# Performance work log

Measured on AMD Instinct MI355X. Metric: run time of the kernel, lower is better.

The kernel has to match this reference:

```python
import jax, jax.numpy as jnp
import numpy as np
from jax import lax

N_IMG = 2
LEVEL_HW = [(200, 200), (100, 100), (50, 50), (25, 25), (13, 13)]
STRIDES = [4, 8, 16, 32, 64]
SIZES = [32.0, 64.0, 128.0, 256.0, 512.0]
A = 3
LEVEL_SIZES = [A * h * w for h, w in LEVEL_HW]
R = sum(LEVEL_SIZES)  # 159882
PRE_NMS = 1000   # pre_nms_top_n['testing']
POST_NMS = 1000  # post_nms_top_n['testing']
NMS_THRESH = 0.7
SCORE_THRESH = 0.0
MIN_SIZE = 1e-3
IMG_H = IMG_W = 800.0
BBOX_XFORM_CLIP = float(np.log(1000.0 / 16.0))


def _make_anchors():
    ratios = np.array([0.5, 1.0, 2.0])
    h_r = np.sqrt(ratios)
    w_r = 1.0 / h_r
    out = []
    for (h, w), stride, size in zip(LEVEL_HW, STRIDES, SIZES):
        ws = size * w_r
        hs = size * h_r
        base = np.stack([-ws / 2, -hs / 2, ws / 2, hs / 2], 1)  # [A,4]
        sx = (np.arange(w) + 0.5) * stride
        sy = (np.arange(h) + 0.5) * stride
        yy, xx = np.meshgrid(sy, sx, indexing='ij')
        shifts = np.stack([xx.ravel(), yy.ravel(), xx.ravel(), yy.ravel()], 1)  # [H*W,4]
        out.append((shifts[:, None, :] + base[None, :, :]).reshape(-1, 4))
    return np.concatenate(out, 0).astype(np.float32)  # [R,4]


def setup_inputs() -> dict:
    key = jax.random.key(0)
    k1, k2 = jax.random.split(key)
    objectness = jax.random.normal(k1, (N_IMG, R), jnp.float32)
    deltas = jax.random.normal(k2, (N_IMG, R, 4), jnp.float32) * 0.2
    anchors = jnp.asarray(_make_anchors())
    return {"objectness": objectness, "deltas": deltas, "anchors": anchors}


def _decode(deltas, anchors):
    # BoxCoder.decode with weights (1,1,1,1)
    wa = anchors[:, 2] - anchors[:, 0]
    ha = anchors[:, 3] - anchors[:, 1]
    cxa = anchors[:, 0] + 0.5 * wa
    cya = anchors[:, 1] + 0.5 * ha
    dx, dy, dw, dh = deltas[..., 0], deltas[..., 1], deltas[..., 2], deltas[..., 3]
    dw = jnp.minimum(dw, BBOX_XFORM_CLIP)
    dh = jnp.minimum(dh, BBOX_XFORM_CLIP)
    cx = dx * wa + cxa
    cy = dy * ha + cya
    w = jnp.exp(dw) * wa
    h = jnp.exp(dh) * ha
    return jnp.stack([cx - 0.5 * w, cy - 0.5 * h, cx + 0.5 * w, cy + 0.5 * h], -1)


def _nms_single(boxes, scores, lvl, valid):
    # batched_nms via per-level coordinate offset trick
    offs = lvl.astype(boxes.dtype) * (max(IMG_H, IMG_W) + 1.0)
    ob = boxes + offs[:, None]
    s = jnp.where(valid, scores, -1.0)
    order = jnp.argsort(-s)
    b = ob[order]          # offset boxes, score-descending
    raw = boxes[order]     # original boxes
    v = valid[order]
    ss = s[order]
    area = (b[:, 2] - b[:, 0]) * (b[:, 3] - b[:, 1])
    lt = jnp.maximum(b[:, None, :2], b[None, :, :2])
    rb = jnp.minimum(b[:, None, 2:], b[None, :, 2:])
    wh = jnp.clip(rb - lt, 0.0)
    inter = wh[..., 0] * wh[..., 1]
    iou = inter / (area[:, None] + area[None, :] - inter + 1e-9)  # [K,K]
    K = b.shape[0]

    def body(keep, i):
        suppressed = jnp.any(keep & (iou[:, i] > NMS_THRESH))
        keep = keep.at[i].set(v[i] & ~suppressed)
        return keep, None

    keep, _ = lax.scan(body, jnp.zeros((K,), bool), jnp.arange(K))
    # compact kept boxes (score order preserved) into fixed POST_NMS slots
    pos = jnp.where(keep, jnp.minimum(jnp.cumsum(keep) - 1, POST_NMS), POST_NMS)
    out_b = jnp.zeros((POST_NMS + 1, 4), boxes.dtype).at[pos].set(raw)[:POST_NMS]
    out_s = jnp.full((POST_NMS + 1,), -1.0, boxes.dtype).at[pos].set(ss)[:POST_NMS]
    return out_b, out_s


def _forward(objectness, deltas, anchors):
    proposals = _decode(deltas, anchors)  # [N,R,4]
    # per-level topk (pre_nms_top_n)
    idxs = []
    off = 0
    for n in LEVEL_SIZES:
        k = min(PRE_NMS, n)
        _, ti = lax.top_k(objectness[:, off:off + n], k)
        idxs.append(ti + off)
        off += n
    top_idx = jnp.concatenate(idxs, 1)  # [N,K]
    obj = jnp.take_along_axis(objectness, top_idx, 1)
    boxes = jnp.take_along_axis(proposals, top_idx[..., None], 1)
    levels = jnp.concatenate([jnp.full((n,), i, jnp.int32) for i, n in enumerate(LEVEL_SIZES)])
    lvl = levels[top_idx]
    scores = jax.nn.sigmoid(obj)
    # clip_boxes_to_image
    x1 = jnp.clip(boxes[..., 0], 0.0, IMG_W)
    y1 = jnp.clip(boxes[..., 1], 0.0, IMG_H)
    x2 = jnp.clip(boxes[..., 2], 0.0, IMG_W)
    y2 = jnp.clip(boxes[..., 3], 0.0, IMG_H)
    boxes = jnp.stack([x1, y1, x2, y2], -1)
    # remove_small_boxes + score_thresh -> validity mask (fixed shapes)
    valid = (x2 - x1 >= MIN_SIZE) & (y2 - y1 >= MIN_SIZE) & (scores >= SCORE_THRESH)
    return jax.vmap(_nms_single)(boxes, scores, lvl, valid)


def reference(objectness, deltas, anchors):
    return _forward(objectness, deltas, anchors)
```

## Files before the change

### kernel.cpp

```cpp
#include <hip/hip_runtime.h>

typedef unsigned long long u64;
typedef unsigned int u32;

#define R_TOT 159882
#define POST 1000
#define IMG_SZ 800.0f
#define NMS_TH 0.7f
#define BBOX_CLIP 4.135166556742356f
#define LCAP 1024

__device__ __forceinline__ float fadd_(float a, float b){ return __fadd_rn(a,b); }
__device__ __forceinline__ float fsub_(float a, float b){ return __fsub_rn(a,b); }
__device__ __forceinline__ float fmul_(float a, float b){ return __fmul_rn(a,b); }

__device__ __forceinline__ int lvl_len(int l){ const int L[5]={120000,30000,7500,1875,507}; return L[l]; }
__device__ __forceinline__ int lvl_off(int l){ const int L[5]={0,120000,150000,157500,159375}; return L[l]; }
__device__ __forceinline__ int lvl_k(int l){ const int L[5]={1000,1000,1000,1000,507}; return L[l]; }

__device__ __forceinline__ u32 mono_(u32 u){ return (u & 0x80000000u) ? ~u : (u | 0x80000000u); }

__device__ __forceinline__ u64 readlane64(u64 v, int i){
  u32 lo = (u32)__builtin_amdgcn_readlane((int)(u32)v, i);
  u32 hi = (u32)__builtin_amdgcn_readlane((int)(u32)(v >> 32), i);
  return ((u64)hi << 32) | (u64)lo;
}

__global__ __launch_bounds__(256) void k_hist(const float* __restrict__ obj, int* hist16){
  int g = blockIdx.x, sl = blockIdx.y;
  int img = g/5, lvl = g%5;
  int n = lvl_len(lvl), s0 = lvl_off(lvl);
  __shared__ int lh[4096];
  int tid = threadIdx.x;
  for (int i = tid; i < 4096; i += 256) lh[i] = 0;
  __syncthreads();
  int lo = (int)((long long)n * sl / 16), hiS = (int)((long long)n * (sl+1) / 16);
  const float* p = obj + img*R_TOT + s0;
  #pragma unroll 4
  for (int e = lo + tid; e < hiS; e += 256){
    u32 mu = mono_(__float_as_uint(p[e]));
    atomicAdd(&lh[(~mu) >> 20], 1);
  }
  __syncthreads();
  int* dst = hist16 + (g*16 + sl)*4096;
  for (int i = tid; i < 4096; i += 256) dst[i] = lh[i];
}

__global__ __launch_bounds__(256) void k_collect(const float* __restrict__ obj,
                                                 const int* __restrict__ hist16,
                                                 u64* mainS, u64* tieS,
                                                 int* cntS, int* cnt2S,
                                                 int* bstarG, int* remG){
  int g = blockIdx.x, sl = blockIdx.y;
  int img = g/5, lvl = g%5;
  int n = lvl_len(lvl), s0 = lvl_off(lvl), k = lvl_k(lvl);
  int tid = threadIdx.x, lane = tid & 63, wid = tid >> 6;
  __shared__ int wsum[4];
  __shared__ int sh_bs, sh_rem, lc, lc2;
  __shared__ u64 lmain[1024];
  __shared__ u64 lbuf2[1024];

  int h[16];
  #pragma unroll
  for (int j = 0; j < 16; j++) h[j] = 0;
  const int* hb = hist16 + g*16*4096 + 16*tid;
  for (int s2 = 0; s2 < 16; s2++){
    const int4* hs = (const int4*)(hb + s2*4096);
    int4 a = hs[0], b = hs[1], c = hs[2], d = hs[3];
    h[0]+=a.x;  h[1]+=a.y;  h[2]+=a.z;  h[3]+=a.w;
    h[4]+=b.x;  h[5]+=b.y;  h[6]+=b.z;  h[7]+=b.w;
    h[8]+=c.x;  h[9]+=c.y;  h[10]+=c.z; h[11]+=c.w;
    h[12]+=d.x; h[13]+=d.y; h[14]+=d.z; h[15]+=d.w;
  }
  int part = 0;
  #pragma unroll
  for (int j = 0; j < 16; j++) part += h[j];
  int x = part;
  for (int d = 1; d < 64; d <<= 1){ int y = __shfl_up(x, d); if (lane >= d) x += y; }
  if (lane == 63) wsum[wid] = x;
  if (tid == 0){ lc = 0; lc2 = 0; }
  __syncthreads();
  int add = 0;
  for (int w = 0; w < wid; w++) add += wsum[w];
  int incl = x + add, excl = incl - part;
  if (excl < k && k <= incl){
    int cum = excl;
    #pragma unroll
    for (int q = 0; q < 16; q++){
      if (cum + h[q] >= k){ sh_bs = 16*tid + q; sh_rem = k - cum; break; }
      cum += h[q];
    }
  }
  __syncthreads();
  int bs = sh_bs;
  if (sl == 0 && tid == 0){ bstarG[g] = bs; remG[g] = sh_rem; }

  int lo = (int)((long long)n * sl / 16), hiS = (int)((long long)n * (sl+1) / 16);
  const float* p = obj + img*R_TOT + s0;
  #pragma unroll 4
  for (int e = lo + tid; e < hiS; e += 256){
    u32 mu = mono_(__float_as_uint(p[e]));
    u64 key56 = (((u64)(~mu)) << 24) | (u32)(s0 + e);
    int bin = (int)(key56 >> 44);
    if (bin < bs){ int pos = atomicAdd(&lc, 1); lmain[pos] = key56; }
    else if (bin == bs){ int pos = atomicAdd(&lc2, 1); if (pos < 1024) lbuf2[pos] = key56; }
  }
  __syncthreads();
  int idx16 = g*16 + sl;
  if (tid == 0){ cntS[idx16] = lc; cnt2S[idx16] = lc2; }
  for (int i = tid; i < lc; i += 256) mainS[idx16*1024 + i] = lmain[i];
  int c2l = lc2 < 1024 ? lc2 : 1024;
  for (int i = tid; i < c2l; i += 256) tieS[idx16*1024 + i] = lbuf2[i];
}

__global__ __launch_bounds__(1024) void k_seldecode(const float* __restrict__ obj,
                                                    const float4* __restrict__ deltas,
                                                    const float4* __restrict__ anchors,
                                                    const u64* __restrict__ mainS,
                                                    const u64* __restrict__ tieS,
                                                    const int* __restrict__ cntS,
                                                    const int* __restrict__ cnt2S,
                                                    const int* __restrict__ remG,
                                                    const int* __restrict__ bstarG,
                                                    float4* boxL, float* scoreL,
                                                    float4* nbox, u64* okeyN, int* ncnt){
  int g = blockIdx.x, img = g/5, lvl = g%5;
  int s0 = lvl_off(lvl), n = lvl_len(lvl), k = lvl_k(lvl);
  const float* p = obj + img*R_TOT + s0;
  __shared__ u64 Lbuf[LCAP];
  __shared__ u64 mainL[1024];
  __shared__ float4 lbox[1024];
  __shared__ u64 lokey[1024];
  __shared__ unsigned char lval[1024];
  __shared__ int h16[16];
  __shared__ int scnt[16], tcnt[16];
  __shared__ int sbase[17], tbase[17];
  __shared__ int sh_sc, sh_rem;
  __shared__ u64 sh_thr;
  int tid = threadIdx.x, lane = tid & 63;
  if (tid < 16){ scnt[tid] = cntS[g*16 + tid]; tcnt[tid] = cnt2S[g*16 + tid]; }
  __syncthreads();
  if (tid == 0){
    int s = 0, t2 = 0;
    #pragma unroll
    for (int q = 0; q < 16; q++){ sbase[q] = s; s += scnt[q]; tbase[q] = t2; t2 += tcnt[q]; }
    sbase[16] = s; tbase[16] = t2;
  }
  __syncthreads();
  int nb = sbase[16];
  int c2 = tbase[16];
  int rem = remG[g];
  int bs = bstarG[g];
  {
    u64 vmain = ~0ull;
    if (tid < nb){
      int sl = 0;
      #pragma unroll
      for (int q = 1; q < 16; q++) sl += (tid >= sbase[q]) ? 1 : 0;
      vmain = mainS[(g*16 + sl)*1024 + (tid - sbase[sl])];
    }
    mainL[tid] = vmain;
  }
  if (tid == 0){ sh_sc = 0; sh_rem = rem; }
  int c2c = c2 < LCAP ? c2 : LCAP;
  for (int e = tid; e < c2c; e += 1024){
    int sl = 0;
    #pragma unroll
    for (int q = 1; q < 16; q++) sl += (e >= tbase[q]) ? 1 : 0;
    Lbuf[e] = tieS[(g*16 + sl)*1024 + (e - tbase[sl])];
  }
  __syncthreads();
  if (c2 <= LCAP){
    for (int e = tid; e < c2; e += 1024){
      u64 kk = Lbuf[e];
      int rk = 0;
      for (int q = 0; q < c2; q++) rk += (Lbuf[q] < kk) ? 1 : 0;
      if (rk < rem){ int p2 = atomicAdd(&sh_sc, 1); mainL[nb + p2] = kk; }
    }
  } else {
    if (tid == 0) sh_thr = ((u64)bs) << 44;
    __syncthreads();
    for (int shift = 40; shift >= 0; shift -= 4){
      if (tid < 16) h16[tid] = 0;
      __syncthreads();
      u64 pref = sh_thr;
      u64 himask = ~((1ull << (shift+4)) - 1ull);
      for (int e = tid; e < n; e += 1024){
        u32 mu = mono_(__float_as_uint(p[e]));
        u64 kk = (((u64)(~mu)) << 24) | (u32)(s0 + e);
        if ((kk & himask) == (pref & himask)) atomicAdd(&h16[(int)((kk >> shift) & 15)], 1);
      }
      __syncthreads();
      if (tid == 0){
        int r2 = sh_rem, cum = 0;
        for (int d = 0; d < 16; d++){
          int hb = h16[d];
          if (cum + hb >= r2){ sh_thr = pref | ((u64)d << shift); sh_rem = r2 - cum; break; }
          cum += hb;
        }
      }
      __syncthreads();
    }
    u64 thr = sh_thr;
    for (int e = tid; e < n; e += 1024){
      u32 mu = mono_(__float_as_uint(p[e]));
      u64 kk = (((u64)(~mu)) << 24) | (u32)(s0 + e);
      if ((int)(kk >> 44) == bs && kk <= thr){ int p2 = atomicAdd(&sh_sc, 1); mainL[nb + p2] = kk; }
    }
  }
  __syncthreads();
  for (int k2 = 2; k2 <= 1024; k2 <<= 1){
    for (int j = k2 >> 1; j > 0; j >>= 1){
      __syncthreads();
      int i = tid, ixj = i ^ j;
      if (ixj > i){
        u64 a = mainL[i], b = mainL[ixj];
        bool up = (i & k2) == 0;
        if ((a > b) == up){ mainL[i] = b; mainL[ixj] = a; }
      }
    }
  }
  __syncthreads();
  int r = tid, t = g*1024 + r;
  if (r < k){
    int idx = (int)(mainL[r] & 0xFFFFFFu);
    float4 a = anchors[idx];
    float4 d = deltas[img*R_TOT + idx];
    float o = obj[img*R_TOT + idx];
    float wa = fsub_(a.z, a.x), ha = fsub_(a.w, a.y);
    float cxa = fadd_(a.x, fmul_(0.5f, wa)), cya = fadd_(a.y, fmul_(0.5f, ha));
    float dw = fminf(d.z, BBOX_CLIP), dh = fminf(d.w, BBOX_CLIP);
    float cx = fadd_(fmul_(d.x, wa), cxa), cy = fadd_(fmul_(d.y, ha), cya);
    float w  = fmul_(expf(dw), wa),        h  = fmul_(expf(dh), ha);
    float x1 = fsub_(cx, fmul_(0.5f, w)), y1 = fsub_(cy, fmul_(0.5f, h));
    float x2 = fadd_(cx, fmul_(0.5f, w)), y2 = fadd_(cy, fmul_(0.5f, h));
    x1 = fminf(fmaxf(x1, 0.0f), IMG_SZ); y1 = fminf(fmaxf(y1, 0.0f), IMG_SZ);
    x2 = fminf(fmaxf(x2, 0.0f), IMG_SZ); y2 = fminf(fmaxf(y2, 0.0f), IMG_SZ);
    bool valid = (fsub_(x2, x1) >= 1e-3f) && (fsub_(y2, y1) >= 1e-3f);
    float e = expf(-o);
    float sig = __fdiv_rn(1.0f, fadd_(1.0f, e));
    float s = valid ? sig : -1.0f;
    u32 sb = __float_as_uint(s);
    u32 ms = (sb & 0x80000000u) ? ~sb : (sb | 0x80000000u);
    float4 b4 = make_float4(x1, y1, x2, y2);
    boxL[t] = b4;
    scoreL[t] = sig;
    lokey[r] = (((u64)(~ms)) << 32) | (u32)(lvl*1000 + r);
    lbox[r] = b4;
    lval[r] = valid ? 1 : 0;
  } else {
    lval[r] = 0;
  }
  __syncthreads();
  if (tid < 64){
    int cnt = 0;
    float off = (float)lvl * 801.0f;
    for (int base = 0; base < k; base += 64){
      int r2 = base + lane;
      bool v = (r2 < k) && lval[r2];
      float4 b = lbox[r2 < k ? r2 : 0];
      u64 mask = __ballot(v);
      int before = __popcll(mask & ((1ull << lane) - 1ull));
      if (v){
        int pos = cnt + before;
        nbox[g*1024 + pos] = make_float4(fadd_(b.x,off), fadd_(b.y,off), fadd_(b.z,off), fadd_(b.w,off));
        okeyN[g*1024 + pos] = lokey[r2];
      }
      cnt += __popcll(mask);
    }
    if (lane == 0) ncnt[g] = cnt;
  }
}

__global__ __launch_bounds__(64) void k_mask(const float4* __restrict__ nbox,
                                             const int* __restrict__ ncnt,
                                             u64* LTG2){
  int g = blockIdx.x, tr = blockIdx.y, tw = blockIdx.z;
  if (tw > tr) return;
  int m = ncnt[g];
  if (tr*64 >= m) return;
  __shared__ float4 shb[64];
  __shared__ float sharea[64];
  int lane = threadIdx.x;
  if (tw*64 + lane < m){
    float4 b = nbox[g*1024 + tw*64 + lane];
    shb[lane] = b;
    sharea[lane] = fmul_(fsub_(b.z,b.x), fsub_(b.w,b.y));
  }
  __syncthreads();
  int j = tr*64 + lane;
  if (j >= m) return;
  float4 a = nbox[g*1024 + j];
  float areaA = fmul_(fsub_(a.z,a.x), fsub_(a.w,a.y));
  int imax = m - tw*64; if (imax > 64) imax = 64;
  if (tw == tr){
    u64 bitsF = 0;
    for (int ii = lane+1; ii < imax; ii++){
      float4 b = shb[ii];
      float ltx = fmaxf(a.x, b.x), lty = fmaxf(a.y, b.y);
      float rbx = fminf(a.z, b.z), rby = fminf(a.w, b.w);
      float wx = fmaxf(fsub_(rbx, ltx), 0.0f), wy = fmaxf(fsub_(rby, lty), 0.0f);
      float inter = fmul_(wx, wy);
      float den = fadd_(fsub_(fadd_(areaA, sharea[ii]), inter), 1e-9f);
      if (__fdiv_rn(inter, den) > NMS_TH) bitsF |= (1ull << ii);
    }
    LTG2[((size_t)(g*1024 + j))*16 + 15] = bitsF;
  } else {
    u64 bits = 0;
    for (int ii = 0; ii < imax; ii++){
      float4 b = shb[ii];
      float ltx = fmaxf(a.x, b.x), lty = fmaxf(a.y, b.y);
      float rbx = fminf(a.z, b.z), rby = fminf(a.w, b.w);
      float wx = fmaxf(fsub_(rbx, ltx), 0.0f), wy = fmaxf(fsub_(rby, lty), 0.0f);
      float inter = fmul_(wx, wy);
      float den = fadd_(fsub_(fadd_(areaA, sharea[ii]), inter), 1e-9f);
      if (__fdiv_rn(inter, den) > NMS_TH) bits |= (1ull << ii);
    }
    LTG2[((size_t)(g*1024 + j))*16 + tw] = bits;
  }
}

struct ChunkBuf {
  ulonglong2 v0, v1, v2, v3, v4, v5, v6, v7;
  u64 ok;
};

__device__ __forceinline__ void issue_chunk(const u64* __restrict__ LT2,
                                            const u64* __restrict__ oK,
                                            int c, int lane, ChunkBuf& b){
  int row = c*64 + lane;
  const ulonglong2* rp = (const ulonglong2*)(LT2 + (size_t)row*16);
  b.v0 = rp[0]; b.v1 = rp[1]; b.v2 = rp[2]; b.v3 = rp[3];
  b.v4 = rp[4]; b.v5 = rp[5]; b.v6 = rp[6]; b.v7 = rp[7];
  b.ok = oK[row];
}

__device__ __forceinline__ void consume_chunk(const ChunkBuf& b, int c, int m, int lane,
                                              u64* KwR, u64* runsL, int& cnt){
  int row = c*64 + lane;
  bool inr = row < m;
  u64 supp = 0;
  #define TERM(q, val) supp |= (((q) < c) ? (val) : 0ull) & KwR[q];
  TERM(0,  b.v0.x) TERM(1,  b.v0.y) TERM(2,  b.v1.x) TERM(3,  b.v1.y)
  TERM(4,  b.v2.x) TERM(5,  b.v2.y) TERM(6,  b.v3.x) TERM(7,  b.v3.y)
  TERM(8,  b.v4.x) TERM(9,  b.v4.y) TERM(10, b.v5.x) TERM(11, b.v5.y)
  TERM(12, b.v6.x) TERM(13, b.v6.y) TERM(14, b.v7.x)
  #undef TERM
  u64 fwd = inr ? b.v7.y : 0;
  u64 live = __ballot(inr && (supp == 0));
  u64 fz = __ballot(fwd != 0);
  u64 kept = 0;
  while (1){
    u64 lf = live & fz;
    if (!lf){ kept |= live; break; }
    int i = __builtin_ctzll(lf);
    u64 bi = 1ull << i;
    u64 below = live & (bi - 1ull);
    kept |= below | bi;
    live &= ~(below | bi);
    live &= ~readlane64(fwd, i);
  }
  KwR[c] = kept;
  bool kp = (kept >> lane) & 1ull;
  int before = __popcll(kept & ((1ull << lane) - 1ull));
  if (kp) runsL[cnt + before] = b.ok;
  cnt += __popcll(kept);
}

__global__ __launch_bounds__(1024) void k_scanmerge(const u64* __restrict__ LTG2,
                                                    const int* __restrict__ ncnt,
                                                    const u64* __restrict__ okeyN,
                                                    const float4* __restrict__ boxL,
                                                    const float* __restrict__ scoreL,
                                                    float* out){
  int img = blockIdx.x, tid = threadIdx.x, lane = tid & 63, wid = tid >> 6;
  __shared__ u64 runs[5*1024];
  __shared__ u64 Kw[5][16];
  __shared__ int cl[5];
  if (wid < 5){
    int l = wid, g = img*5 + l;
    int m = ncnt[g];
    int nch = (m + 63) >> 6;
    const u64* LT2 = LTG2 + ((size_t)g*1024)*16;
    const u64* oK = okeyN + g*1024;
    u64* KwR = &Kw[l][0];
    u64* runsL = &runs[l*1024];
    int cnt = 0;
    ChunkBuf A, B;
    if (nch > 0){
      issue_chunk(LT2, oK, 0, lane, A);
      int c = 0;
      while (c < nch){
        if (c+1 < nch) issue_chunk(LT2, oK, c+1, lane, B);
        consume_chunk(A, c, m, lane, KwR, runsL, cnt);
        c++;
        if (c >= nch) break;
        if (c+1 < nch) issue_chunk(LT2, oK, c+1, lane, A);
        consume_chunk(B, c, m, lane, KwR, runsL, cnt);
        c++;
      }
    }
    if (lane == 0) cl[l] = cnt;
  } else {
    for (int t = tid - 320; t < POST; t += 704){
      out[img*POST*4 + t*4 + 0] = 0.0f;
      out[img*POST*4 + t*4 + 1] = 0.0f;
      out[img*POST*4 + t*4 + 2] = 0.0f;
      out[img*POST*4 + t*4 + 3] = 0.0f;
      out[2*POST*4 + img*POST + t] = -1.0f;
    }
  }
  __syncthreads();
  for (int idx = tid; idx < 5*1024; idx += 1024){
    int l = idx >> 10, i = idx & 1023;
    if (i < cl[l]){
      u64 key = runs[l*1024 + i];
      int o0 = l+1; if (o0 >= 5) o0 -= 5;
      int o1 = l+2; if (o1 >= 5) o1 -= 5;
      int o2 = l+3; if (o2 >= 5) o2 -= 5;
      int o3 = l+4; if (o3 >= 5) o3 -= 5;
      const u64* r0 = runs + (o0 << 10);
      const u64* r1 = runs + (o1 << 10);
      const u64* r2 = runs + (o2 << 10);
      const u64* r3 = runs + (o3 << 10);
      int lo0 = 0, hi0 = cl[o0];
      int lo1 = 0, hi1 = cl[o1];
      int lo2 = 0, hi2 = cl[o2];
      int lo3 = 0, hi3 = cl[o3];
      #pragma unroll 1
      for (int st = 0; st < 11; st++){
        int m0 = (lo0+hi0)>>1, m1 = (lo1+hi1)>>1, m2 = (lo2+hi2)>>1, m3 = (lo3+hi3)>>1;
        u64 a0 = r0[m0], a1 = r1[m1], a2 = r2[m2], a3 = r3[m3];
        if (lo0 < hi0){ if (a0 < key) lo0 = m0+1; else hi0 = m0; }
        if (lo1 < hi1){ if (a1 < key) lo1 = m1+1; else hi1 = m1; }
        if (lo2 < hi2){ if (a2 < key) lo2 = m2+1; else hi2 = m2; }
        if (lo3 < hi3){ if (a3 < key) lo3 = m3+1; else hi3 = m3; }
      }
      int rank = i + lo0 + lo1 + lo2 + lo3;
      if (rank < POST){
        int pos = (int)(key & 0xFFFFFFFFull);
        int lvl = pos / 1000, r = pos - lvl*1000;
        int gg = img*5 + lvl;
        float4 bo = boxL[gg*1024 + r];
        float sc = scoreL[gg*1024 + r];
        out[img*POST*4 + rank*4 + 0] = bo.x;
        out[img*POST*4 + rank*4 + 1] = bo.y;
        out[img*POST*4 + rank*4 + 2] = bo.z;
        out[img*POST*4 + rank*4 + 3] = bo.w;
        out[2*POST*4 + img*POST + rank] = sc;
      }
    }
  }
}

extern "C" void kernel_launch(void* const* d_in, const int* in_sizes, int n_in,
                              void* d_out, int out_size, void* d_ws, size_t ws_size,
                              hipStream_t stream){
  (void)in_sizes; (void)n_in; (void)out_size; (void)ws_size;
  const float*  obj     = (const float*)d_in[0];
  const float4* deltas  = (const float4*)d_in[1];
  const float4* anchors = (const float4*)d_in[2];
  float* out = (float*)d_out;
  char* ws = (char*)d_ws;
  int* hist16  = (int*)(ws + 0);
  u64* mainS   = (u64*)(ws + 2621440);
  u64* tieS    = (u64*)(ws + 3932160);
  int* cntS    = (int*)(ws + 5242880);
  int* cnt2S   = (int*)(ws + 5243520);
  int* bstarG  = (int*)(ws + 5244160);
  int* remG    = (int*)(ws + 5244224);
  float4* boxL = (float4*)(ws + 5244288);
  float* scoreL= (float*)(ws + 5408128);
  u64* okeyN   = (u64*)(ws + 5449088);
  float4* nbox = (float4*)(ws + 5531008);
  u64* LTG2    = (u64*)(ws + 5694848);
  int* ncnt    = (int*)(ws + 7005568);

  {
    dim3 gh(10, 16);
    k_hist<<<gh, 256, 0, stream>>>(obj, hist16);
  }
  {
    dim3 gc(10, 16);
    k_collect<<<gc, 256, 0, stream>>>(obj, hist16, mainS, tieS, cntS, cnt2S, bstarG, remG);
  }
  k_seldecode<<<10, 1024, 0, stream>>>(obj, deltas, anchors, mainS, tieS, cntS, cnt2S,
                                       remG, bstarG, boxL, scoreL, nbox, okeyN, ncnt);
  {
    dim3 gm(10, 16, 16);
    k_mask<<<gm, 64, 0, stream>>>(nbox, ncnt, LTG2);
  }
  k_scanmerge<<<2, 1024, 0, stream>>>(LTG2, ncnt, okeyN, boxL, scoreL, out);
}
```

Before: 157.7 us.

## Fuse histogram and collect kernels using per-slice local top-k threshold

Merges k_hist and k_collect into a single k_front kernel. Each slice now picks its own threshold bin from its local histogram, keeping its top min(k, slice size) candidates, so no global histogram round trip through memory is needed. k_seldecode then re-histograms the gathered candidates to find the global bin and remainder. It falls back to a full-level radix select when tie buffers overflow. This removes a kernel launch and the 16x4096 histogram write and read, at the cost of more candidates per level being moved and sorted in the select kernel.

```diff
diff --git a/kernel.cpp b/kernel.cpp
--- a/kernel.cpp
+++ b/kernel.cpp
@@ -26,15 +26,21 @@
   return ((u64)hi << 32) | (u64)lo;
 }
 
-__global__ __launch_bounds__(256) void k_hist(const float* __restrict__ obj, int* hist16){
+__global__ __launch_bounds__(256) void k_front(const float* __restrict__ obj,
+                                               u64* mainS, u64* tieS,
+                                               int* cntS, int* cnt2S){
   int g = blockIdx.x, sl = blockIdx.y;
   int img = g/5, lvl = g%5;
-  int n = lvl_len(lvl), s0 = lvl_off(lvl);
-  __shared__ int lh[4096];
-  int tid = threadIdx.x;
+  int n = lvl_len(lvl), s0 = lvl_off(lvl), k = lvl_k(lvl);
+  int tid = threadIdx.x, lane = tid & 63, wid = tid >> 6;
+  __shared__ __align__(16) int lh[4096];
+  __shared__ int wsum[4];
+  __shared__ int sh_bs, lc, lc2;
   for (int i = tid; i < 4096; i += 256) lh[i] = 0;
   __syncthreads();
   int lo = (int)((long long)n * sl / 16), hiS = (int)((long long)n * (sl+1) / 16);
+  int ns = hiS - lo;
+  int ks = k < ns ? k : ns;
   const float* p = obj + img*R_TOT + s0;
   #pragma unroll 4
   for (int e = lo + tid; e < hiS; e += 256){
@@ -42,36 +48,9 @@
     atomicAdd(&lh[(~mu) >> 20], 1);
   }
   __syncthreads();
-  int* dst = hist16 + (g*16 + sl)*4096;
-  for (int i = tid; i < 4096; i += 256) dst[i] = lh[i];
-}
-
-__global__ __launch_bounds__(256) void k_collect(const float* __restrict__ obj,
-                                                 const int* __restrict__ hist16,
-                                                 u64* mainS, u64* tieS,
-                                                 int* cntS, int* cnt2S,
-                                                 int* bstarG, int* remG){
-  int g = blockIdx.x, sl = blockIdx.y;
-  int img = g/5, lvl = g%5;
-  int n = lvl_len(lvl), s0 = lvl_off(lvl), k = lvl_k(lvl);
-  int tid = threadIdx.x, lane = tid & 63, wid = tid >> 6;
-  __shared__ int wsum[4];
-  __shared__ int sh_bs, sh_rem, lc, lc2;
-  __shared__ u64 lmain[1024];
-  __shared__ u64 lbuf2[1024];
-
   int h[16];
   #pragma unroll
-  for (int j = 0; j < 16; j++) h[j] = 0;
-  const int* hb = hist16 + g*16*4096 + 16*tid;
-  for (int s2 = 0; s2 < 16; s2++){
-    const int4* hs = (const int4*)(hb + s2*4096);
-    int4 a = hs[0], b = hs[1], c = hs[2], d = hs[3];
-    h[0]+=a.x;  h[1]+=a.y;  h[2]+=a.z;  h[3]+=a.w;
-    h[4]+=b.x;  h[5]+=b.y;  h[6]+=b.z;  h[7]+=b.w;
-    h[8]+=c.x;  h[9]+=c.y;  h[10]+=c.z; h[11]+=c.w;
-    h[12]+=d.x; h[13]+=d.y; h[14]+=d.z; h[15]+=d.w;
-  }
+  for (int j = 0; j < 16; j++) h[j] = lh[16*tid + j];
   int part = 0;
   #pragma unroll
   for (int j = 0; j < 16; j++) part += h[j];
@@ -83,34 +62,32 @@
   int add = 0;
   for (int w = 0; w < wid; w++) add += wsum[w];
   int incl = x + add, excl = incl - part;
-  if (excl < k && k <= incl){
+  if (excl < ks && ks <= incl){
     int cum = excl;
     #pragma unroll
     for (int q = 0; q < 16; q++){
-      if (cum + h[q] >= k){ sh_bs = 16*tid + q; sh_rem = k - cum; break; }
+      if (cum + h[q] >= ks){ sh_bs = 16*tid + q; break; }
       cum += h[q];
     }
   }
   __syncthreads();
   int bs = sh_bs;
-  if (sl == 0 && tid == 0){ bstarG[g] = bs; remG[g] = sh_rem; }
-
-  int lo = (int)((long long)n * sl / 16), hiS = (int)((long long)n * (sl+1) / 16);
-  const float* p = obj + img*R_TOT + s0;
+  u64* lmain = (u64*)lh;
+  u64* ltie  = (u64*)lh + 1024;
   #pragma unroll 4
   for (int e = lo + tid; e < hiS; e += 256){
     u32 mu = mono_(__float_as_uint(p[e]));
     u64 key56 = (((u64)(~mu)) << 24) | (u32)(s0 + e);
     int bin = (int)(key56 >> 44);
     if (bin < bs){ int pos = atomicAdd(&lc, 1); lmain[pos] = key56; }
-    else if (bin == bs){ int pos = atomicAdd(&lc2, 1); if (pos < 1024) lbuf2[pos] = key56; }
+    else if (bin == bs){ int pos = atomicAdd(&lc2, 1); if (pos < 1024) ltie[pos] = key56; }
   }
   __syncthreads();
   int idx16 = g*16 + sl;
   if (tid == 0){ cntS[idx16] = lc; cnt2S[idx16] = lc2; }
   for (int i = tid; i < lc; i += 256) mainS[idx16*1024 + i] = lmain[i];
   int c2l = lc2 < 1024 ? lc2 : 1024;
-  for (int i = tid; i < c2l; i += 256) tieS[idx16*1024 + i] = lbuf2[i];
+  for (int i = tid; i < c2l; i += 256) tieS[idx16*1024 + i] = ltie[i];
 }
 
 __global__ __launch_bounds__(1024) void k_seldecode(const float* __restrict__ obj,
@@ -120,8 +97,6 @@
                                                     const u64* __restrict__ tieS,
                                                     const int* __restrict__ cntS,
                                                     const int* __restrict__ cnt2S,
-                                                    const int* __restrict__ remG,
-                                                    const int* __restrict__ bstarG,
                                                     float4* boxL, float* scoreL,
                                                     float4* nbox, u64* okeyN, int* ncnt){
   int g = blockIdx.x, img = g/5, lvl = g%5;
@@ -129,56 +104,146 @@
   const float* p = obj + img*R_TOT + s0;
   __shared__ u64 Lbuf[LCAP];
   __shared__ u64 mainL[1024];
-  __shared__ float4 lbox[1024];
+  __shared__ __align__(16) float4 lbox[1024];
   __shared__ u64 lokey[1024];
   __shared__ unsigned char lval[1024];
   __shared__ int h16[16];
   __shared__ int scnt[16], tcnt[16];
   __shared__ int sbase[17], tbase[17];
-  __shared__ int sh_sc, sh_rem;
+  __shared__ int wsum16[16];
+  __shared__ int sh_bs, sh_rem, sh_mc, sh_tc, sh_sc, sh_rem2, sh_ovf;
   __shared__ u64 sh_thr;
-  int tid = threadIdx.x, lane = tid & 63;
+  int tid = threadIdx.x, lane = tid & 63, wid = tid >> 6;
+  int* chist = (int*)lbox;
   if (tid < 16){ scnt[tid] = cntS[g*16 + tid]; tcnt[tid] = cnt2S[g*16 + tid]; }
+  for (int i = tid; i < 4096; i += 1024) chist[i] = 0;
   __syncthreads();
   if (tid == 0){
-    int s = 0, t2 = 0;
+    int s = 0, t2 = 0, o = 0;
     #pragma unroll
-    for (int q = 0; q < 16; q++){ sbase[q] = s; s += scnt[q]; tbase[q] = t2; t2 += tcnt[q]; }
+    for (int q = 0; q < 16; q++){
+      sbase[q] = s; s += scnt[q];
+      int tc = tcnt[q] < 1024 ? tcnt[q] : 1024;
+      tbase[q] = t2; t2 += tc;
+      if (tcnt[q] > 1024) o = 1;
+    }
     sbase[16] = s; tbase[16] = t2;
-  }
-  __syncthreads();
-  int nb = sbase[16];
-  int c2 = tbase[16];
-  int rem = remG[g];
-  int bs = bstarG[g];
-  {
-    u64 vmain = ~0ull;
-    if (tid < nb){
-      int sl = 0;
+    sh_ovf = o; sh_mc = 0; sh_tc = 0; sh_sc = 0;
+  }
+  __syncthreads();
+  if (!sh_ovf){
+    int totM = sbase[16], totT = tbase[16];
+    for (int r = tid; r < totM; r += 1024){
+      int s = 0;
       #pragma unroll
-      for (int q = 1; q < 16; q++) sl += (tid >= sbase[q]) ? 1 : 0;
-      vmain = mainS[(g*16 + sl)*1024 + (tid - sbase[sl])];
-    }
-    mainL[tid] = vmain;
-  }
-  if (tid == 0){ sh_sc = 0; sh_rem = rem; }
-  int c2c = c2 < LCAP ? c2 : LCAP;
-  for (int e = tid; e < c2c; e += 1024){
-    int sl = 0;
-    #pragma unroll
-    for (int q = 1; q < 16; q++) sl += (e >= tbase[q]) ? 1 : 0;
-    Lbuf[e] = tieS[(g*16 + sl)*1024 + (e - tbase[sl])];
-  }
-  __syncthreads();
-  if (c2 <= LCAP){
-    for (int e = tid; e < c2; e += 1024){
-      u64 kk = Lbuf[e];
-      int rk = 0;
-      for (int q = 0; q < c2; q++) rk += (Lbuf[q] < kk) ? 1 : 0;
-      if (rk < rem){ int p2 = atomicAdd(&sh_sc, 1); mainL[nb + p2] = kk; }
-    }
-  } else {
-    if (tid == 0) sh_thr = ((u64)bs) << 44;
+      for (int q = 1; q < 16; q++) s += (r >= sbase[q]) ? 1 : 0;
+      u64 kk = mainS[(g*16 + s)*1024 + (r - sbase[s])];
+      atomicAdd(&chist[(int)(kk >> 44)], 1);
+    }
+    for (int r = tid; r < totT; r += 1024){
+      int s = 0;
+      #pragma unroll
+      for (int q = 1; q < 16; q++) s += (r >= tbase[q]) ? 1 : 0;
+      u64 kk = tieS[(g*16 + s)*1024 + (r - tbase[s])];
+      atomicAdd(&chist[(int)(kk >> 44)], 1);
+    }
+    __syncthreads();
+    int h0 = chist[4*tid], h1 = chist[4*tid+1], h2 = chist[4*tid+2], h3 = chist[4*tid+3];
+    int part = h0 + h1 + h2 + h3;
+    int x = part;
+    for (int d = 1; d < 64; d <<= 1){ int y = __shfl_up(x, d); if (lane >= d) x += y; }
+    if (lane == 63) wsum16[wid] = x;
+    __syncthreads();
+    int add = 0;
+    for (int w = 0; w < wid; w++) add += wsum16[w];
+    int incl = x + add, excl = incl - part;
+    if (excl < k && k <= incl){
+      int cum = excl;
+      if (cum + h0 >= k){ sh_bs = 4*tid;   sh_rem = k - cum; }
+      else { cum += h0;
+        if (cum + h1 >= k){ sh_bs = 4*tid+1; sh_rem = k - cum; }
+        else { cum += h1;
+          if (cum + h2 >= k){ sh_bs = 4*tid+2; sh_rem = k - cum; }
+          else { cum += h2;    sh_bs = 4*tid+3; sh_rem = k - cum; }
+        }
+      }
+    }
+    mainL[tid] = ~0ull;
+    __syncthreads();
+    int bs = sh_bs;
+    for (int r = tid; r < totM; r += 1024){
+      int s = 0;
+      #pragma unroll
+      for (int q = 1; q < 16; q++) s += (r >= sbase[q]) ? 1 : 0;
+      u64 kk = mainS[(g*16 + s)*1024 + (r - sbase[s])];
+      int bin = (int)(kk >> 44);
+      if (bin < bs){ int pos = atomicAdd(&sh_mc, 1); mainL[pos] = kk; }
+      else if (bin == bs){ int pos = atomicAdd(&sh_tc, 1); if (pos < LCAP) Lbuf[pos] = kk; }
+    }
+    for (int r = tid; r < totT; r += 1024){
+      int s = 0;
+      #pragma unroll
+      for (int q = 1; q < 16; q++) s += (r >= tbase[q]) ? 1 : 0;
+      u64 kk = tieS[(g*16 + s)*1024 + (r - tbase[s])];
+      int bin = (int)(kk >> 44);
+      if (bin < bs){ int pos = atomicAdd(&sh_mc, 1); mainL[pos] = kk; }
+      else if (bin == bs){ int pos = atomicAdd(&sh_tc, 1); if (pos < LCAP) Lbuf[pos] = kk; }
+    }
+    __syncthreads();
+    int nb = sh_mc, c2r = sh_tc, rem = sh_rem;
+    if (c2r <= LCAP){
+      for (int e = tid; e < c2r; e += 1024){
+        u64 kk = Lbuf[e];
+        int rk = 0;
+        for (int qq = 0; qq < c2r; qq++) rk += (Lbuf[qq] < kk) ? 1 : 0;
+        if (rk < rem){ int p2 = atomicAdd(&sh_sc, 1); mainL[nb + p2] = kk; }
+      }
+    } else {
+      if (tid == 0) sh_ovf = 1;
+    }
+    __syncthreads();
+  }
+  if (sh_ovf){
+    int* fh = (int*)lbox;
+    for (int i = tid; i < 4096; i += 1024) fh[i] = 0;
+    if (tid == 0){ sh_mc = 0; sh_sc = 0; }
+    __syncthreads();
+    for (int e = tid; e < n; e += 1024){
+      u32 mu = mono_(__float_as_uint(p[e]));
+      atomicAdd(&fh[(int)((~mu) >> 20)], 1);
+    }
+    __syncthreads();
+    int h0 = fh[4*tid], h1 = fh[4*tid+1], h2 = fh[4*tid+2], h3 = fh[4*tid+3];
+    int part = h0 + h1 + h2 + h3;
+    int x = part;
+    for (int d = 1; d < 64; d <<= 1){ int y = __shfl_up(x, d); if (lane >= d) x += y; }
+    if (lane == 63) wsum16[wid] = x;
+    __syncthreads();
+    int add = 0;
+    for (int w = 0; w < wid; w++) add += wsum16[w];
+    int incl = x + add, excl = incl - part;
+    if (excl < k && k <= incl){
+      int cum = excl;
+      if (cum + h0 >= k){ sh_bs = 4*tid;   sh_rem = k - cum; }
+      else { cum += h0;
+        if (cum + h1 >= k){ sh_bs = 4*tid+1; sh_rem = k - cum; }
+        else { cum += h1;
+          if (cum + h2 >= k){ sh_bs = 4*tid+2; sh_rem = k - cum; }
+          else { cum += h2;    sh_bs = 4*tid+3; sh_rem = k - cum; }
+        }
+      }
+    }
+    mainL[tid] = ~0ull;
+    __syncthreads();
+    int bs = sh_bs;
+    for (int e = tid; e < n; e += 1024){
+      u32 mu = mono_(__float_as_uint(p[e]));
+      u64 kk = (((u64)(~mu)) << 24) | (u32)(s0 + e);
+      if ((int)(kk >> 44) < bs){ int pos = atomicAdd(&sh_mc, 1); mainL[pos] = kk; }
+    }
+    __syncthreads();
+    int nb = sh_mc;
+    if (tid == 0){ sh_thr = ((u64)bs) << 44; sh_rem2 = sh_rem; }
     __syncthreads();
     for (int shift = 40; shift >= 0; shift -= 4){
       if (tid < 16) h16[tid] = 0;
@@ -192,11 +257,11 @@
       }
       __syncthreads();
       if (tid == 0){
-        int r2 = sh_rem, cum = 0;
+        int r2 = sh_rem2, cum = 0;
         for (int d = 0; d < 16; d++){
-          int hb = h16[d];
-          if (cum + hb >= r2){ sh_thr = pref | ((u64)d << shift); sh_rem = r2 - cum; break; }
-          cum += hb;
+          int hb2 = h16[d];
+          if (cum + hb2 >= r2){ sh_thr = pref | ((u64)d << shift); sh_rem2 = r2 - cum; break; }
+          cum += hb2;
         }
       }
       __syncthreads();
@@ -207,8 +272,8 @@
       u64 kk = (((u64)(~mu)) << 24) | (u32)(s0 + e);
       if ((int)(kk >> 44) == bs && kk <= thr){ int p2 = atomicAdd(&sh_sc, 1); mainL[nb + p2] = kk; }
     }
-  }
-  __syncthreads();
+    __syncthreads();
+  }
   for (int k2 = 2; k2 <= 1024; k2 <<= 1){
     for (int j = k2 >> 1; j > 0; j >>= 1){
       __syncthreads();
@@ -462,30 +527,23 @@
   const float4* anchors = (const float4*)d_in[2];
   float* out = (float*)d_out;
   char* ws = (char*)d_ws;
-  int* hist16  = (int*)(ws + 0);
-  u64* mainS   = (u64*)(ws + 2621440);
-  u64* tieS    = (u64*)(ws + 3932160);
-  int* cntS    = (int*)(ws + 5242880);
-  int* cnt2S   = (int*)(ws + 5243520);
-  int* bstarG  = (int*)(ws + 5244160);
-  int* remG    = (int*)(ws + 5244224);
-  float4* boxL = (float4*)(ws + 5244288);
-  float* scoreL= (float*)(ws + 5408128);
-  u64* okeyN   = (u64*)(ws + 5449088);
-  float4* nbox = (float4*)(ws + 5531008);
-  u64* LTG2    = (u64*)(ws + 5694848);
-  int* ncnt    = (int*)(ws + 7005568);
+  u64* mainS   = (u64*)(ws + 0);
+  u64* tieS    = (u64*)(ws + 1310720);
+  int* cntS    = (int*)(ws + 2621440);
+  int* cnt2S   = (int*)(ws + 2622080);
+  float4* boxL = (float4*)(ws + 2622720);
+  float* scoreL= (float*)(ws + 2786560);
+  u64* okeyN   = (u64*)(ws + 2827520);
+  float4* nbox = (float4*)(ws + 2909440);
+  u64* LTG2    = (u64*)(ws + 3073280);
+  int* ncnt    = (int*)(ws + 4384000);
 
   {
-    dim3 gh(10, 16);
-    k_hist<<<gh, 256, 0, stream>>>(obj, hist16);
-  }
-  {
-    dim3 gc(10, 16);
-    k_collect<<<gc, 256, 0, stream>>>(obj, hist16, mainS, tieS, cntS, cnt2S, bstarG, remG);
+    dim3 gf(10, 16);
+    k_front<<<gf, 256, 0, stream>>>(obj, mainS, tieS, cntS, cnt2S);
   }
   k_seldecode<<<10, 1024, 0, stream>>>(obj, deltas, anchors, mainS, tieS, cntS, cnt2S,
-                                       remG, bstarG, boxL, scoreL, nbox, okeyN, ncnt);
+                                       boxL, scoreL, nbox, okeyN, ncnt);
   {
     dim3 gm(10, 16, 16);
     k_mask<<<gm, 64, 0, stream>>>(nbox, ncnt, LTG2);
```

After: 170.2 us. 7.9% more time.
